# Performance work log

Measured on AMD Instinct MI355X. Metric: run time of the kernel, lower is better.

Reference implementation:

```python
import jax, jax.numpy as jnp
import numpy as np

S, T, B = 32, 64, 64          # sentences, tokens/sentence, batch
V, E, H, G, C = 32000, 128, 128, 128, 5  # vocab, embed, intra hid, inter hid, classes


def _gru_dir(x, h0, Wih, Whh, bih, bhh):
    # x: [T,B,D]; Wih: [3H,D]; Whh: [3H,H]  (PyTorch GRU gate order r,z,n)
    xg = jnp.einsum('tbd,gd->tbg', x, Wih) + bih  # precompute input gates [T,B,3H]
    def step(h, xt):
        gh = h @ Whh.T + bhh
        ir, iz, inn = jnp.split(xt, 3, axis=-1)
        hr, hz, hn = jnp.split(gh, 3, axis=-1)
        r = jax.nn.sigmoid(ir + hr)
        z = jax.nn.sigmoid(iz + hz)
        n = jnp.tanh(inn + r * hn)
        hnew = (1 - z) * n + z * h
        return hnew, hnew
    _, out = jax.lax.scan(step, h0, xg)
    return out  # [T,B,H]


def _bigru(x, Wih, Whh, bih, bhh):
    # x: [T,B,D]; Wih: [2,3H,D] (fwd, bwd). Zero initial state (init_hidden()).
    h0 = jnp.zeros((x.shape[1], Whh.shape[-1]), x.dtype)
    of = _gru_dir(x, h0, Wih[0], Whh[0], bih[0], bhh[0])
    ob = _gru_dir(x[::-1], h0, Wih[1], Whh[1], bih[1], bhh[1])[::-1]
    return jnp.concatenate([of, ob], axis=-1)  # [T,B,2H]


def setup_inputs() -> dict:
    key = jax.random.key(0)
    ks = iter(jax.random.split(key, 20))
    u = lambda k, shp, s: jax.random.uniform(k, shp, jnp.float32, -s, s)
    tokens = jax.random.randint(next(ks), (S, T, B), 0, V)
    return {
        'tokens': tokens,
        'embed_table': jax.random.normal(next(ks), (V, E), jnp.float32),
        # intra biGRU (input E, hidden H)
        'Wih_intra': u(next(ks), (2, 3 * H, E), 0.08),
        'Whh_intra': u(next(ks), (2, 3 * H, H), 0.08),
        'bih_intra': u(next(ks), (2, 3 * H), 0.08),
        'bhh_intra': u(next(ks), (2, 3 * H), 0.08),
        # intra attention
        'W_W_intra': u(next(ks), (2 * H, 2 * H), 0.1),
        'b_intra': u(next(ks), (2 * H,), 0.1),
        'proj_intra': u(next(ks), (2 * H,), 0.1),
        # inter biGRU (input 2H, hidden G)
        'Wih_inter': u(next(ks), (2, 3 * G, 2 * H), 0.08),
        'Whh_inter': u(next(ks), (2, 3 * G, G), 0.08),
        'bih_inter': u(next(ks), (2, 3 * G), 0.08),
        'bhh_inter': u(next(ks), (2, 3 * G), 0.08),
        # inter attention
        'W_W_inter': u(next(ks), (2 * G, 2 * G), 0.1),
        'b_inter': u(next(ks), (2 * G,), 0.1),
        'proj_inter': u(next(ks), (2 * G,), 0.1),
        # final linear
        'W_final': u(next(ks), (C, 2 * G), 0.06),
        'b_final': u(next(ks), (C,), 0.06),
    }


def reference(tokens, embed_table, Wih_intra, Whh_intra, bih_intra, bhh_intra,
              W_W_intra, b_intra, proj_intra, Wih_inter, Whh_inter, bih_inter,
              bhh_inter, W_W_inter, b_inter, proj_inter, W_final, b_final):
    # ---- intra (word-level) per sentence, fresh zero state each sentence ----
    emb = embed_table[tokens]                                   # [S,T,B,E]
    intra_out = jax.vmap(
        lambda xs: _bigru(xs, Wih_intra, Whh_intra, bih_intra, bhh_intra)
    )(emb)                                                      # [S,T,B,2H]
    u1 = jnp.tanh(jnp.einsum('stbh,hk->stbk', intra_out, W_W_intra) + b_intra)
    a1 = jnp.einsum('stbk,k->stb', u1, proj_intra)              # [S,T,B]
    a1 = jax.nn.softmax(a1, axis=1)                             # softmax over tokens
    sent_vecs = jnp.einsum('stb,stbh->sbh', a1, intra_out)      # [S,B,2H]
    # ---- inter (sentence-level) ----
    inter_out = _bigru(sent_vecs, Wih_inter, Whh_inter, bih_inter, bhh_inter)  # [S,B,2G]
    u2 = jnp.tanh(jnp.einsum('sbh,hk->sbk', inter_out, W_W_inter) + b_inter)
    a2 = jnp.einsum('sbk,k->sb', u2, proj_inter)                # NO softmax (faithful to source)
    doc_vec = jnp.einsum('sb,sbh->bh', a2, inter_out)           # [B,2G]
    final_map = doc_vec @ W_final.T + b_final                   # [B,C]
    return final_map
```

## Files before the change

kernel.cpp:

```cpp
#include <hip/hip_runtime.h>

#define S_ 32
#define T_ 64
#define B_ 64
#define V_ 32000
#define E_ 128
#define H_ 128
#define G_ 128
#define C_ 5

typedef short s8v __attribute__((ext_vector_type(8)));
typedef __bf16 b8v __attribute__((ext_vector_type(8)));
typedef float f32x4 __attribute__((ext_vector_type(4)));

template <typename V>
__device__ inline auto mfma_sel(V a, V b, f32x4 c, int)
    -> decltype(__builtin_amdgcn_mfma_f32_16x16x32_bf16(a, b, c, 0, 0, 0)) {
  return __builtin_amdgcn_mfma_f32_16x16x32_bf16(a, b, c, 0, 0, 0);
}
template <typename V>
__device__ inline f32x4 mfma_sel(V a, V b, f32x4 c, long) {
  return __builtin_amdgcn_mfma_f32_16x16x32_bf16(
      __builtin_bit_cast(b8v, a), __builtin_bit_cast(b8v, b), c, 0, 0, 0);
}
__device__ inline f32x4 mfma16(s8v a, s8v b, f32x4 c) { return mfma_sel(a, b, c, 0); }

__device__ inline float b2f(unsigned short u) {
  union { unsigned int i; float f; } v; v.i = ((unsigned int)u) << 16; return v.f;
}
__device__ inline unsigned short f2b(float f) {
  union { float f; unsigned int i; } v; v.f = f;
  return (unsigned short)((v.i + 0x8000u) >> 16);
}
__device__ inline unsigned short f2b_rne(float f) {
  union { float f; unsigned int i; } v; v.f = f;
  unsigned int r = (v.i + 0x7fffu + ((v.i >> 16) & 1u)) >> 16;
  return (unsigned short)r;
}
__device__ inline s8v cvt8(const float* p) {
  const float4 a = *(const float4*)p;
  const float4 b = *(const float4*)(p + 4);
  s8v r;
  r[0] = (short)f2b_rne(a.x); r[1] = (short)f2b_rne(a.y);
  r[2] = (short)f2b_rne(a.z); r[3] = (short)f2b_rne(a.w);
  r[4] = (short)f2b_rne(b.x); r[5] = (short)f2b_rne(b.y);
  r[6] = (short)f2b_rne(b.z); r[7] = (short)f2b_rne(b.w);
  return r;
}
__device__ inline float fsigm(float x) {
  return __builtin_amdgcn_rcpf(1.f + __builtin_amdgcn_exp2f(-1.44269504f * x));
}
__device__ inline float ftanh(float x) {
  return 1.f - 2.f * __builtin_amdgcn_rcpf(1.f + __builtin_amdgcn_exp2f(2.88539008f * x));
}

__device__ inline void lds_barrier() {
  asm volatile("s_waitcnt lgkmcnt(0)\n\ts_barrier" ::: "memory");
}

__global__ __launch_bounds__(256) void k_gtab(
    const float* __restrict__ emb,
    const float* __restrict__ wih,
    const float* __restrict__ bih,
    const float* __restrict__ bhh,
    const float* __restrict__ wwi,
    unsigned short* __restrict__ gtab,
    unsigned short* __restrict__ wta)
{
  __shared__ __align__(16) unsigned short smem[64 * 264];
  const int bid = blockIdx.x, tid = threadIdx.x;
  if (bid >= 3000) {
    const int n0 = (bid - 3000) * 64;
    for (int i = 0; i < 64; ++i) {
      int cid = i * 256 + tid;
      int k = cid >> 6, nl = cid & 63;
      smem[nl * 264 + k] = f2b_rne(wwi[k * 256 + n0 + nl]);
    }
    __syncthreads();
    for (int i = 0; i < 8; ++i) {
      int cid = i * 256 + tid;
      int nl = cid >> 5, k8 = cid & 31;
      *(int4*)&wta[(size_t)(n0 + nl) * 256 + k8 * 8] =
          *(const int4*)&smem[nl * 264 + k8 * 8];
    }
    return;
  }
  const int mchunk = bid / 6, nchunk = bid % 6;
  const int vbase = mchunk * 64, nbase = nchunk * 128;
  for (int i = 0; i < 8; ++i) {
    int cid = i * 256 + tid;
    int row = cid >> 5, kc = cid & 31;
    float4 v = *(const float4*)&emb[(size_t)(vbase + row) * 128 + kc * 4];
    ushort4 u;
    u.x = f2b_rne(v.x); u.y = f2b_rne(v.y); u.z = f2b_rne(v.z); u.w = f2b_rne(v.w);
    *(ushort4*)&smem[row * 136 + kc * 4] = u;
  }
  __syncthreads();
  const int w = tid >> 6, l = tid & 63, q = l >> 4, ln = l & 15;
  s8v bf[2][4];
  float bias[2];
  for (int nt = 0; nt < 2; ++nt) {
    int c = nbase + (w * 2 + nt) * 16 + ln;
    int g = (c < 384) ? c : (c - 384);
    bias[nt] = bih[c] + (g < 256 ? bhh[c] : 0.f);
    for (int kf = 0; kf < 4; ++kf)
      bf[nt][kf] = cvt8(&wih[(size_t)c * 128 + kf * 32 + q * 8]);
  }
  for (int mt = 0; mt < 4; ++mt) {
    s8v af[4];
    for (int kf = 0; kf < 4; ++kf)
      af[kf] = *(const s8v*)&smem[(mt * 16 + ln) * 136 + kf * 32 + q * 8];
    for (int nt = 0; nt < 2; ++nt) {
      f32x4 acc = {0.f, 0.f, 0.f, 0.f};
      for (int kf = 0; kf < 4; ++kf) acc = mfma16(af[kf], bf[nt][kf], acc);
      const int col = nbase + (w * 2 + nt) * 16 + ln;
      for (int r = 0; r < 4; ++r) {
        const int row = vbase + mt * 16 + q * 4 + r;
        gtab[(size_t)row * 768 + col] = f2b_rne(acc[r] + bias[nt]);
      }
    }
  }
}

__global__ __launch_bounds__(512) void k_intra(
    const int* __restrict__ tokens,
    const unsigned short* __restrict__ gtab,
    const float* __restrict__ whh,
    const float* __restrict__ bhh,
    unsigned short* __restrict__ iout)
{
  const int bid = blockIdx.x;
  const int s = bid >> 3, dir = (bid >> 2) & 1, bq = bid & 3;
  const int bbase = bq * 16;
  const int tid = threadIdx.x;
  const int w = tid >> 6, l = tid & 63, q = l >> 4, ln = l & 15;
  const int gbase = w * 16, g0 = gbase + q * 4;

  __shared__ __align__(16) unsigned short hb[2][16 * 136];
  __shared__ int tokl[T_ * 16];

  for (int i = tid; i < 2 * 16 * 136; i += 512) ((unsigned short*)hb)[i] = 0;
  for (int i = tid; i < T_ * 16; i += 512) {
    int t = i >> 4, bl = i & 15;
    tokl[i] = tokens[(s * T_ + t) * B_ + bbase + bl];
  }

  s8v af[3][4];
  float hbn[4];
  const float* whd = whh + (size_t)dir * (384 * 128);
  const float* bhd = bhh + dir * 384;
  for (int g3 = 0; g3 < 3; ++g3) {
    const int R = g3 * 128 + gbase;
    for (int kf = 0; kf < 4; ++kf)
      af[g3][kf] = cvt8(&whd[(size_t)(R + ln) * 128 + kf * 32 + q * 8]);
  }
  for (int r = 0; r < 4; ++r) hbn[r] = bhd[256 + gbase + q * 4 + r];
  float h[4] = {0.f, 0.f, 0.f, 0.f};
  const int b = bbase + ln;
  __syncthreads();

  const int tfirst = dir ? (T_ - 1) : 0;
  const unsigned short* gr0 =
      gtab + (size_t)tokl[tfirst * 16 + ln] * 768 + dir * 384 + g0;
  ushort4 xr = *(const ushort4*)&gr0[0];
  ushort4 xz = *(const ushort4*)&gr0[128];
  ushort4 xn = *(const ushort4*)&gr0[256];

  int p = 0;
  for (int step = 0; step < T_; ++step) {
    const int t = dir ? (T_ - 1 - step) : step;
    const int t1 = dir ? (t > 0 ? t - 1 : 0) : (t < T_ - 1 ? t + 1 : T_ - 1);
    const unsigned short* grn =
        gtab + (size_t)tokl[t1 * 16 + ln] * 768 + dir * 384 + g0;
    const ushort4 xrn = *(const ushort4*)&grn[0];
    const ushort4 xzn = *(const ushort4*)&grn[128];
    const ushort4 xnn = *(const ushort4*)&grn[256];

    s8v bfr[4];
    for (int kf = 0; kf < 4; ++kf)
      bfr[kf] = *(const s8v*)&hb[p][ln * 136 + kf * 32 + q * 8];
    f32x4 c0 = {0.f, 0.f, 0.f, 0.f}, c1 = c0, c2 = c0;
    for (int kf = 0; kf < 4; ++kf) {
      c0 = mfma16(af[0][kf], bfr[kf], c0);
      c1 = mfma16(af[1][kf], bfr[kf], c1);
      c2 = mfma16(af[2][kf], bfr[kf], c2);
    }

    const unsigned short* xrp = (const unsigned short*)&xr;
    const unsigned short* xzp = (const unsigned short*)&xz;
    const unsigned short* xnp = (const unsigned short*)&xn;
    unsigned short hnb[4];
    for (int r = 0; r < 4; ++r) {
      float rr = fsigm(b2f(xrp[r]) + c0[r]);
      float zz = fsigm(b2f(xzp[r]) + c1[r]);
      float nn = ftanh(b2f(xnp[r]) + rr * (c2[r] + hbn[r]));
      float hv = zz * (h[r] - nn) + nn;
      h[r] = hv;
      hnb[r] = f2b(hv);
    }
    ushort4 hv4; hv4.x = hnb[0]; hv4.y = hnb[1]; hv4.z = hnb[2]; hv4.w = hnb[3];
    *(ushort4*)&hb[p ^ 1][ln * 136 + g0] = hv4;
    *(ushort4*)&iout[((size_t)(s * T_ + t) * B_ + b) * 256 + dir * 128 + g0] = hv4;
    lds_barrier();
    p ^= 1;
    xr = xrn; xz = xzn; xn = xnn;
  }
}

__global__ __launch_bounds__(512, 1) void k_attn(
    const unsigned short* __restrict__ iout,
    const unsigned short* __restrict__ wta,
    const float* __restrict__ bint,
    const float* __restrict__ proj,
    float* __restrict__ sv)
{
  __shared__ __align__(16) unsigned short wlds[256 * 256];
  __shared__ float lgbuf[8][16];
  __shared__ float lbuf[8][8];
  const int tid = threadIdx.x, bid = blockIdx.x;
  const int s = bid >> 3, b0 = (bid & 7) * 8;
  for (int i = 0; i < 16; ++i) {
    int cid = i * 512 + tid;
    int n = cid >> 5, kc = cid & 31;
    *(int4*)&wlds[n * 256 + ((kc ^ (n & 15)) << 3)] =
        *(const int4*)&wta[(size_t)n * 256 + kc * 8];
  }
  const int w = tid >> 6, l = tid & 63, q = l >> 4, ln = l & 15;
  float bbv[16], ppv[16];
  for (int nt = 0; nt < 16; ++nt) {
    bbv[nt] = bint[nt * 16 + ln];
    ppv[nt] = proj[nt * 16 + ln];
  }
  __syncthreads();

  float O[8][8];
  for (int kf = 0; kf < 8; ++kf)
    for (int j = 0; j < 8; ++j) O[kf][j] = 0.f;
  float l_acc = 0.f;

  for (int tile = 0; tile < 4; ++tile) {
    const int t = (w * 4 + tile) * 2 + (ln >> 3);
    const size_t row = (size_t)((s * T_ + t) * B_ + b0 + (ln & 7));
    s8v af[8];
    for (int kf = 0; kf < 8; ++kf)
      af[kf] = *(const s8v*)&iout[row * 256 + kf * 32 + q * 8];
    float p0 = 0.f, p1 = 0.f, p2 = 0.f, p3 = 0.f;
    for (int nt = 0; nt < 16; ++nt) {
      f32x4 c = {0.f, 0.f, 0.f, 0.f};
      for (int kf = 0; kf < 8; ++kf) {
        s8v bf = *(const s8v*)&wlds[(nt * 16 + ln) * 256 + (((kf * 4 + q) ^ ln) << 3)];
        c = mfma16(af[kf], bf, c);
      }
      p0 += ppv[nt] * ftanh(c[0] + bbv[nt]);
      p1 += ppv[nt] * ftanh(c[1] + bbv[nt]);
      p2 += ppv[nt] * ftanh(c[2] + bbv[nt]);
      p3 += ppv[nt] * ftanh(c[3] + bbv[nt]);
    }
    for (int d = 1; d < 16; d <<= 1) {
      p0 += __shfl_xor(p0, d); p1 += __shfl_xor(p1, d);
      p2 += __shfl_xor(p2, d); p3 += __shfl_xor(p3, d);
    }
    if (ln == 0) {
      lgbuf[w][q * 4 + 0] = p0; lgbuf[w][q * 4 + 1] = p1;
      lgbuf[w][q * 4 + 2] = p2; lgbuf[w][q * 4 + 3] = p3;
    }
    const float lg = lgbuf[w][ln];
    const float e = __builtin_amdgcn_exp2f(1.44269504f * lg);
    l_acc += e;
    for (int kf = 0; kf < 8; ++kf)
      for (int j = 0; j < 8; ++j)
        O[kf][j] += e * b2f((unsigned short)af[kf][j]);
  }
  l_acc += __shfl_xor(l_acc, 8);
  for (int kf = 0; kf < 8; ++kf)
    for (int j = 0; j < 8; ++j) O[kf][j] += __shfl_xor(O[kf][j], 8);
  __syncthreads();
  float* obuf = (float*)wlds;
  if (ln < 8) {
    const int base = w * 2048 + ln * 256 + q * 8;
    for (int kf = 0; kf < 8; ++kf) {
      float4 v0; v0.x = O[kf][0]; v0.y = O[kf][1]; v0.z = O[kf][2]; v0.w = O[kf][3];
      float4 v1; v1.x = O[kf][4]; v1.y = O[kf][5]; v1.z = O[kf][6]; v1.w = O[kf][7];
      *(float4*)&obuf[base + kf * 32]     = v0;
      *(float4*)&obuf[base + kf * 32 + 4] = v1;
    }
    if (q == 0) lbuf[w][ln] = l_acc;
  }
  __syncthreads();
  const int idx = tid * 4;
  const int bb_ = idx >> 8;
  float4 acc; acc.x = 0.f; acc.y = 0.f; acc.z = 0.f; acc.w = 0.f;
  float lsum = 0.f;
  for (int w8 = 0; w8 < 8; ++w8) {
    const float4 v = *(const float4*)&obuf[w8 * 2048 + idx];
    acc.x += v.x; acc.y += v.y; acc.z += v.z; acc.w += v.w;
    lsum += lbuf[w8][bb_];
  }
  const float inv = __builtin_amdgcn_rcpf(lsum);
  float4 r; r.x = acc.x * inv; r.y = acc.y * inv; r.z = acc.z * inv; r.w = acc.w * inv;
  *(float4*)&sv[(size_t)((s * B_ + b0 + bb_) * 256) + (idx & 255)] = r;
}

__global__ __launch_bounds__(256) void k_xgi(
    const float* __restrict__ sv,
    const float* __restrict__ wihI,
    const float* __restrict__ bihI,
    const float* __restrict__ bhhI,
    float* __restrict__ xgi)
{
  const int bid = blockIdx.x, tid = threadIdx.x;
  const int r0 = bid * 8;
  __shared__ float svl[8 * 256];
  for (int i = 0; i < 8; ++i) svl[i * 256 + tid] = sv[(size_t)(r0 + i) * 256 + tid];
  __syncthreads();
  for (int cc = 0; cc < 3; ++cc) {
    const int c = cc * 256 + tid;
    const int dir = c / 384, g = c - dir * 384;
    const float bias = bihI[c] + (g < 256 ? bhhI[c] : 0.f);
    float acc[8];
    for (int i = 0; i < 8; ++i) acc[i] = bias;
    const float* wr = wihI + (size_t)c * 256;
    for (int hh = 0; hh < 256; ++hh) {
      const float wv = wr[hh];
      for (int i = 0; i < 8; ++i) acc[i] += wv * svl[i * 256 + hh];
    }
    for (int i = 0; i < 8; ++i)
      xgi[((size_t)dir * 2048 + r0 + i) * 384 + g] = acc[i];
  }
}

__global__ __launch_bounds__(512) void k_inter(
    const float* __restrict__ xgi,
    const float* __restrict__ whh,
    const float* __restrict__ bhh,
    float* __restrict__ io2)
{
  const int bid = blockIdx.x;
  const int dir = bid >> 2, bq = bid & 3, bbase = bq * 16;
  const int tid = threadIdx.x;
  const int w = tid >> 6, l = tid & 63, q = l >> 4, ln = l & 15;
  const int gbase = w * 16, g0 = gbase + q * 4;
  __shared__ __align__(16) unsigned short hb[2][16 * 136];
  for (int i = tid; i < 2 * 16 * 136; i += 512) ((unsigned short*)hb)[i] = 0;
  s8v af[3][4];
  float hbn[4];
  const float* whd = whh + (size_t)dir * (384 * 128);
  const float* bhd = bhh + dir * 384;
  for (int g3 = 0; g3 < 3; ++g3) {
    const int R = g3 * 128 + gbase;
    for (int kf = 0; kf < 4; ++kf)
      af[g3][kf] = cvt8(&whd[(size_t)(R + ln) * 128 + kf * 32 + q * 8]);
  }
  for (int r = 0; r < 4; ++r) hbn[r] = bhd[256 + gbase + q * 4 + r];
  float h[4] = {0.f, 0.f, 0.f, 0.f};
  const int b = bbase + ln;
  __syncthreads();

  const int sfirst = dir ? (S_ - 1) : 0;
  const float* xp0 = xgi + ((size_t)dir * 2048 + sfirst * 64 + b) * 384 + g0;
  float4 vr = *(const float4*)&xp0[0];
  float4 vz = *(const float4*)&xp0[128];
  float4 vn = *(const float4*)&xp0[256];

  int p = 0;
  for (int step = 0; step < S_; ++step) {
    const int sI = dir ? (S_ - 1 - step) : step;
    const int s1 = dir ? (sI > 0 ? sI - 1 : 0) : (sI < S_ - 1 ? sI + 1 : S_ - 1);
    const float* xpn = xgi + ((size_t)dir * 2048 + s1 * 64 + b) * 384 + g0;
    const float4 vrn = *(const float4*)&xpn[0];
    const float4 vzn = *(const float4*)&xpn[128];
    const float4 vnn = *(const float4*)&xpn[256];

    s8v bfr[4];
    for (int kf = 0; kf < 4; ++kf)
      bfr[kf] = *(const s8v*)&hb[p][ln * 136 + kf * 32 + q * 8];
    f32x4 c0 = {0.f, 0.f, 0.f, 0.f}, c1 = c0, c2 = c0;
    for (int kf = 0; kf < 4; ++kf) {
      c0 = mfma16(af[0][kf], bfr[kf], c0);
      c1 = mfma16(af[1][kf], bfr[kf], c1);
      c2 = mfma16(af[2][kf], bfr[kf], c2);
    }
    const float irv[4] = {vr.x, vr.y, vr.z, vr.w};
    const float izv[4] = {vz.x, vz.y, vz.z, vz.w};
    const float inv[4] = {vn.x, vn.y, vn.z, vn.w};
    unsigned short hnb[4];
    for (int r = 0; r < 4; ++r) {
      float rr = fsigm(irv[r] + c0[r]);
      float zz = fsigm(izv[r] + c1[r]);
      float nn = ftanh(inv[r] + rr * (c2[r] + hbn[r]));
      float hv = zz * (h[r] - nn) + nn;
      h[r] = hv;
      hnb[r] = f2b(hv);
    }
    ushort4 hv4; hv4.x = hnb[0]; hv4.y = hnb[1]; hv4.z = hnb[2]; hv4.w = hnb[3];
    *(ushort4*)&hb[p ^ 1][ln * 136 + g0] = hv4;
    float4 of4; of4.x = h[0]; of4.y = h[1]; of4.z = h[2]; of4.w = h[3];
    *(float4*)&io2[((size_t)(sI * 64 + b)) * 256 + dir * 128 + g0] = of4;
    lds_barrier();
    p ^= 1;
    vr = vrn; vz = vzn; vn = vnn;
  }
}

__global__ __launch_bounds__(256) void k_attn_i(
    const float* __restrict__ io2,
    const float* __restrict__ wwI,
    const float* __restrict__ bI,
    const float* __restrict__ projI,
    float* __restrict__ a2)
{
  const int bid = blockIdx.x, tid = threadIdx.x;
  const int r0 = bid * 8;
  __shared__ float iol[8 * 256];
  __shared__ float red[4 * 8];
  for (int i = 0; i < 8; ++i) iol[i * 256 + tid] = io2[(size_t)(r0 + i) * 256 + tid];
  __syncthreads();
  float acc[8];
  for (int i = 0; i < 8; ++i) acc[i] = 0.f;
  for (int hh = 0; hh < 256; ++hh) {
    const float wv = wwI[hh * 256 + tid];
    for (int i = 0; i < 8; ++i) acc[i] += wv * iol[i * 256 + hh];
  }
  const float bb = bI[tid], pp = projI[tid];
  float p[8];
  for (int i = 0; i < 8; ++i) p[i] = pp * ftanh(acc[i] + bb);
  for (int d = 1; d < 64; d <<= 1)
    for (int i = 0; i < 8; ++i) p[i] += __shfl_xor(p[i], d);
  const int w = tid >> 6, l = tid & 63;
  if (l == 0)
    for (int i = 0; i < 8; ++i) red[w * 8 + i] = p[i];
  __syncthreads();
  if (tid < 8) a2[r0 + tid] = red[tid] + red[8 + tid] + red[16 + tid] + red[24 + tid];
}

__global__ __launch_bounds__(256) void k_final(
    const float* __restrict__ a2,
    const float* __restrict__ io2,
    const float* __restrict__ wf,
    const float* __restrict__ bfi,
    float* __restrict__ out)
{
  const int b = blockIdx.x, tid = threadIdx.x;
  __shared__ float av[S_];
  __shared__ float dv[256];
  __shared__ float red[4];
  if (tid < S_) av[tid] = a2[tid * 64 + b];
  __syncthreads();
  float acc = 0.f;
  for (int s = 0; s < S_; ++s) acc += av[s] * io2[((size_t)(s * 64 + b)) * 256 + tid];
  dv[tid] = acc;
  __syncthreads();
  for (int c = 0; c < C_; ++c) {
    float pv = wf[c * 256 + tid] * dv[tid];
    for (int d = 1; d < 64; d <<= 1) pv += __shfl_xor(pv, d);
    const int w = tid >> 6, l = tid & 63;
    if (l == 0) red[w] = pv;
    __syncthreads();
    if (tid == 0)
      out[b * C_ + c] = red[0] + red[1] + red[2] + red[3] + bfi[c];
    __syncthreads();
  }
}

extern "C" void kernel_launch(void* const* d_in, const int* in_sizes, int n_in,
                              void* d_out, int out_size, void* d_ws, size_t ws_size,
                              hipStream_t stream) {
  (void)in_sizes; (void)n_in; (void)out_size; (void)ws_size;
  const int*   tokens = (const int*)d_in[0];
  const float* emb    = (const float*)d_in[1];
  const float* wih_a  = (const float*)d_in[2];
  const float* whh_a  = (const float*)d_in[3];
  const float* bih_a  = (const float*)d_in[4];
  const float* bhh_a  = (const float*)d_in[5];
  const float* ww_a   = (const float*)d_in[6];
  const float* b_a    = (const float*)d_in[7];
  const float* proj_a = (const float*)d_in[8];
  const float* wih_i  = (const float*)d_in[9];
  const float* whh_i  = (const float*)d_in[10];
  const float* bih_i  = (const float*)d_in[11];
  const float* bhh_i  = (const float*)d_in[12];
  const float* ww_i   = (const float*)d_in[13];
  const float* b_i    = (const float*)d_in[14];
  const float* proj_i = (const float*)d_in[15];
  const float* w_fin  = (const float*)d_in[16];
  const float* b_fin  = (const float*)d_in[17];

  char* ws = (char*)d_ws;
  unsigned short* gtab = (unsigned short*)(ws + 0);
  unsigned short* wta  = (unsigned short*)(ws + 49152000);
  unsigned short* iout = (unsigned short*)(ws + 49283072);
  float* sv  = (float*)(ws + 117440512);
  float* xgi = (float*)(ws + 119537664);
  float* io2 = (float*)(ws + 125829120);
  float* a2  = (float*)(ws + 127926272);

  k_gtab<<<3004, 256, 0, stream>>>(emb, wih_a, bih_a, bhh_a, ww_a, gtab, wta);
  k_intra<<<256, 512, 0, stream>>>(tokens, gtab, whh_a, bhh_a, iout);
  k_attn<<<256, 512, 0, stream>>>(iout, wta, b_a, proj_a, sv);
  k_xgi<<<256, 256, 0, stream>>>(sv, wih_i, bih_i, bhh_i, xgi);
  k_inter<<<8, 512, 0, stream>>>(xgi, whh_i, bhh_i, io2);
  k_attn_i<<<256, 256, 0, stream>>>(io2, ww_i, b_i, proj_i, a2);
  k_final<<<64, 256, 0, stream>>>(a2, io2, w_fin, b_fin, (float*)d_out);
}
```

Measured before the change: 338.5 us.

## Deepen gate prefetch in GRU recurrences and reuse embedding tile across gate chunks

The intra and inter GRU recurrences now prefetch the input-gate rows two steps ahead through a four-slot register ring, using a 4x unrolled loop. This is meant to hide the latency of the gathered gtab/xgi loads behind more than one recurrence step. Separately, k_gtab has each block load and convert its 64-row embedding tile once and loop over all six output column chunks, which cuts the grid from 3004 to 504 blocks and avoids reloading the embedding tile six times. The cost is more registers in the recurrent kernels and less parallelism in the table build.

```diff
diff --git a/kernel.cpp b/kernel.cpp
--- a/kernel.cpp
+++ b/kernel.cpp
@@ -69,8 +69,8 @@
 {
   __shared__ __align__(16) unsigned short smem[64 * 264];
   const int bid = blockIdx.x, tid = threadIdx.x;
-  if (bid >= 3000) {
-    const int n0 = (bid - 3000) * 64;
+  if (bid >= 500) {
+    const int n0 = (bid - 500) * 64;
     for (int i = 0; i < 64; ++i) {
       int cid = i * 256 + tid;
       int k = cid >> 6, nl = cid & 63;
@@ -85,8 +85,7 @@
     }
     return;
   }
-  const int mchunk = bid / 6, nchunk = bid % 6;
-  const int vbase = mchunk * 64, nbase = nchunk * 128;
+  const int vbase = bid * 64;
   for (int i = 0; i < 8; ++i) {
     int cid = i * 256 + tid;
     int row = cid >> 5, kc = cid & 31;
@@ -97,26 +96,30 @@
   }
   __syncthreads();
   const int w = tid >> 6, l = tid & 63, q = l >> 4, ln = l & 15;
-  s8v bf[2][4];
-  float bias[2];
-  for (int nt = 0; nt < 2; ++nt) {
-    int c = nbase + (w * 2 + nt) * 16 + ln;
-    int g = (c < 384) ? c : (c - 384);
-    bias[nt] = bih[c] + (g < 256 ? bhh[c] : 0.f);
+  s8v af[4][4];
+  for (int mt = 0; mt < 4; ++mt)
     for (int kf = 0; kf < 4; ++kf)
-      bf[nt][kf] = cvt8(&wih[(size_t)c * 128 + kf * 32 + q * 8]);
-  }
-  for (int mt = 0; mt < 4; ++mt) {
-    s8v af[4];
-    for (int kf = 0; kf < 4; ++kf)
-      af[kf] = *(const s8v*)&smem[(mt * 16 + ln) * 136 + kf * 32 + q * 8];
+      af[mt][kf] = *(const s8v*)&smem[(mt * 16 + ln) * 136 + kf * 32 + q * 8];
+  for (int nchunk = 0; nchunk < 6; ++nchunk) {
+    const int nbase = nchunk * 128;
+    s8v bf[2][4];
+    float bias[2];
     for (int nt = 0; nt < 2; ++nt) {
-      f32x4 acc = {0.f, 0.f, 0.f, 0.f};
-      for (int kf = 0; kf < 4; ++kf) acc = mfma16(af[kf], bf[nt][kf], acc);
-      const int col = nbase + (w * 2 + nt) * 16 + ln;
-      for (int r = 0; r < 4; ++r) {
-        const int row = vbase + mt * 16 + q * 4 + r;
-        gtab[(size_t)row * 768 + col] = f2b_rne(acc[r] + bias[nt]);
+      int c = nbase + (w * 2 + nt) * 16 + ln;
+      int g = (c < 384) ? c : (c - 384);
+      bias[nt] = bih[c] + (g < 256 ? bhh[c] : 0.f);
+      for (int kf = 0; kf < 4; ++kf)
+        bf[nt][kf] = cvt8(&wih[(size_t)c * 128 + kf * 32 + q * 8]);
+    }
+    for (int mt = 0; mt < 4; ++mt) {
+      for (int nt = 0; nt < 2; ++nt) {
+        f32x4 acc = {0.f, 0.f, 0.f, 0.f};
+        for (int kf = 0; kf < 4; ++kf) acc = mfma16(af[mt][kf], bf[nt][kf], acc);
+        const int col = nbase + (w * 2 + nt) * 16 + ln;
+        for (int r = 0; r < 4; ++r) {
+          const int row = vbase + mt * 16 + q * 4 + r;
+          gtab[(size_t)row * 768 + col] = f2b_rne(acc[r] + bias[nt]);
+        }
       }
     }
   }
@@ -159,52 +162,59 @@
   const int b = bbase + ln;
   __syncthreads();
 
-  const int tfirst = dir ? (T_ - 1) : 0;
-  const unsigned short* gr0 =
-      gtab + (size_t)tokl[tfirst * 16 + ln] * 768 + dir * 384 + g0;
-  ushort4 xr = *(const ushort4*)&gr0[0];
-  ushort4 xz = *(const ushort4*)&gr0[128];
-  ushort4 xn = *(const ushort4*)&gr0[256];
+  ushort4 Xr[4], Xz[4], Xn[4];
+#define GLOAD_I(slot, st)                                                   \
+  do {                                                                      \
+    int tt_ = (st) > (T_ - 1) ? (T_ - 1) : (st);                            \
+    int tg_ = dir ? (T_ - 1 - tt_) : tt_;                                   \
+    const unsigned short* gp_ =                                             \
+        gtab + (size_t)tokl[tg_ * 16 + ln] * 768 + dir * 384 + g0;          \
+    Xr[slot] = *(const ushort4*)&gp_[0];                                    \
+    Xz[slot] = *(const ushort4*)&gp_[128];                                  \
+    Xn[slot] = *(const ushort4*)&gp_[256];                                  \
+  } while (0)
+
+  GLOAD_I(0, 0);
+  GLOAD_I(1, 1);
 
   int p = 0;
-  for (int step = 0; step < T_; ++step) {
-    const int t = dir ? (T_ - 1 - step) : step;
-    const int t1 = dir ? (t > 0 ? t - 1 : 0) : (t < T_ - 1 ? t + 1 : T_ - 1);
-    const unsigned short* grn =
-        gtab + (size_t)tokl[t1 * 16 + ln] * 768 + dir * 384 + g0;
-    const ushort4 xrn = *(const ushort4*)&grn[0];
-    const ushort4 xzn = *(const ushort4*)&grn[128];
-    const ushort4 xnn = *(const ushort4*)&grn[256];
-
-    s8v bfr[4];
-    for (int kf = 0; kf < 4; ++kf)
-      bfr[kf] = *(const s8v*)&hb[p][ln * 136 + kf * 32 + q * 8];
-    f32x4 c0 = {0.f, 0.f, 0.f, 0.f}, c1 = c0, c2 = c0;
-    for (int kf = 0; kf < 4; ++kf) {
-      c0 = mfma16(af[0][kf], bfr[kf], c0);
-      c1 = mfma16(af[1][kf], bfr[kf], c1);
-      c2 = mfma16(af[2][kf], bfr[kf], c2);
-    }
-
-    const unsigned short* xrp = (const unsigned short*)&xr;
-    const unsigned short* xzp = (const unsigned short*)&xz;
-    const unsigned short* xnp = (const unsigned short*)&xn;
-    unsigned short hnb[4];
-    for (int r = 0; r < 4; ++r) {
-      float rr = fsigm(b2f(xrp[r]) + c0[r]);
-      float zz = fsigm(b2f(xzp[r]) + c1[r]);
-      float nn = ftanh(b2f(xnp[r]) + rr * (c2[r] + hbn[r]));
-      float hv = zz * (h[r] - nn) + nn;
-      h[r] = hv;
-      hnb[r] = f2b(hv);
-    }
-    ushort4 hv4; hv4.x = hnb[0]; hv4.y = hnb[1]; hv4.z = hnb[2]; hv4.w = hnb[3];
-    *(ushort4*)&hb[p ^ 1][ln * 136 + g0] = hv4;
-    *(ushort4*)&iout[((size_t)(s * T_ + t) * B_ + b) * 256 + dir * 128 + g0] = hv4;
-    lds_barrier();
-    p ^= 1;
-    xr = xrn; xz = xzn; xn = xnn;
-  }
+  for (int it = 0; it < T_ / 4; ++it) {
+#pragma unroll
+    for (int j = 0; j < 4; ++j) {
+      const int step = it * 4 + j;
+      const int t = dir ? (T_ - 1 - step) : step;
+      GLOAD_I((j + 2) & 3, step + 2);
+
+      s8v bfr[4];
+      for (int kf = 0; kf < 4; ++kf)
+        bfr[kf] = *(const s8v*)&hb[p][ln * 136 + kf * 32 + q * 8];
+      f32x4 c0 = {0.f, 0.f, 0.f, 0.f}, c1 = c0, c2 = c0;
+      for (int kf = 0; kf < 4; ++kf) {
+        c0 = mfma16(af[0][kf], bfr[kf], c0);
+        c1 = mfma16(af[1][kf], bfr[kf], c1);
+        c2 = mfma16(af[2][kf], bfr[kf], c2);
+      }
+
+      const unsigned short* xrp = (const unsigned short*)&Xr[j];
+      const unsigned short* xzp = (const unsigned short*)&Xz[j];
+      const unsigned short* xnp = (const unsigned short*)&Xn[j];
+      unsigned short hnb[4];
+      for (int r = 0; r < 4; ++r) {
+        float rr = fsigm(b2f(xrp[r]) + c0[r]);
+        float zz = fsigm(b2f(xzp[r]) + c1[r]);
+        float nn = ftanh(b2f(xnp[r]) + rr * (c2[r] + hbn[r]));
+        float hv = zz * (h[r] - nn) + nn;
+        h[r] = hv;
+        hnb[r] = f2b(hv);
+      }
+      ushort4 hv4; hv4.x = hnb[0]; hv4.y = hnb[1]; hv4.z = hnb[2]; hv4.w = hnb[3];
+      *(ushort4*)&hb[p ^ 1][ln * 136 + g0] = hv4;
+      *(ushort4*)&iout[((size_t)(s * T_ + t) * B_ + b) * 256 + dir * 128 + g0] = hv4;
+      lds_barrier();
+      p ^= 1;
+    }
+  }
+#undef GLOAD_I
 }
 
 __global__ __launch_bounds__(512, 1) void k_attn(
@@ -356,50 +366,58 @@
   const int b = bbase + ln;
   __syncthreads();
 
-  const int sfirst = dir ? (S_ - 1) : 0;
-  const float* xp0 = xgi + ((size_t)dir * 2048 + sfirst * 64 + b) * 384 + g0;
-  float4 vr = *(const float4*)&xp0[0];
-  float4 vz = *(const float4*)&xp0[128];
-  float4 vn = *(const float4*)&xp0[256];
+  float4 Vr[4], Vz[4], Vn[4];
+#define GLOAD_S(slot, st)                                                   \
+  do {                                                                      \
+    int tt_ = (st) > (S_ - 1) ? (S_ - 1) : (st);                            \
+    int sg_ = dir ? (S_ - 1 - tt_) : tt_;                                   \
+    const float* xp_ = xgi + ((size_t)dir * 2048 + sg_ * 64 + b) * 384 + g0;\
+    Vr[slot] = *(const float4*)&xp_[0];                                     \
+    Vz[slot] = *(const float4*)&xp_[128];                                   \
+    Vn[slot] = *(const float4*)&xp_[256];                                   \
+  } while (0)
+
+  GLOAD_S(0, 0);
+  GLOAD_S(1, 1);
 
   int p = 0;
-  for (int step = 0; step < S_; ++step) {
-    const int sI = dir ? (S_ - 1 - step) : step;
-    const int s1 = dir ? (sI > 0 ? sI - 1 : 0) : (sI < S_ - 1 ? sI + 1 : S_ - 1);
-    const float* xpn = xgi + ((size_t)dir * 2048 + s1 * 64 + b) * 384 + g0;
-    const float4 vrn = *(const float4*)&xpn[0];
-    const float4 vzn = *(const float4*)&xpn[128];
-    const float4 vnn = *(const float4*)&xpn[256];
-
-    s8v bfr[4];
-    for (int kf = 0; kf < 4; ++kf)
-      bfr[kf] = *(const s8v*)&hb[p][ln * 136 + kf * 32 + q * 8];
-    f32x4 c0 = {0.f, 0.f, 0.f, 0.f}, c1 = c0, c2 = c0;
-    for (int kf = 0; kf < 4; ++kf) {
-      c0 = mfma16(af[0][kf], bfr[kf], c0);
-      c1 = mfma16(af[1][kf], bfr[kf], c1);
-      c2 = mfma16(af[2][kf], bfr[kf], c2);
-    }
-    const float irv[4] = {vr.x, vr.y, vr.z, vr.w};
-    const float izv[4] = {vz.x, vz.y, vz.z, vz.w};
-    const float inv[4] = {vn.x, vn.y, vn.z, vn.w};
-    unsigned short hnb[4];
-    for (int r = 0; r < 4; ++r) {
-      float rr = fsigm(irv[r] + c0[r]);
-      float zz = fsigm(izv[r] + c1[r]);
-      float nn = ftanh(inv[r] + rr * (c2[r] + hbn[r]));
-      float hv = zz * (h[r] - nn) + nn;
-      h[r] = hv;
-      hnb[r] = f2b(hv);
-    }
-    ushort4 hv4; hv4.x = hnb[0]; hv4.y = hnb[1]; hv4.z = hnb[2]; hv4.w = hnb[3];
-    *(ushort4*)&hb[p ^ 1][ln * 136 + g0] = hv4;
-    float4 of4; of4.x = h[0]; of4.y = h[1]; of4.z = h[2]; of4.w = h[3];
-    *(float4*)&io2[((size_t)(sI * 64 + b)) * 256 + dir * 128 + g0] = of4;
-    lds_barrier();
-    p ^= 1;
-    vr = vrn; vz = vzn; vn = vnn;
-  }
+  for (int it = 0; it < S_ / 4; ++it) {
+#pragma unroll
+    for (int j = 0; j < 4; ++j) {
+      const int step = it * 4 + j;
+      const int sI = dir ? (S_ - 1 - step) : step;
+      GLOAD_S((j + 2) & 3, step + 2);
+
+      s8v bfr[4];
+      for (int kf = 0; kf < 4; ++kf)
+        bfr[kf] = *(const s8v*)&hb[p][ln * 136 + kf * 32 + q * 8];
+      f32x4 c0 = {0.f, 0.f, 0.f, 0.f}, c1 = c0, c2 = c0;
+      for (int kf = 0; kf < 4; ++kf) {
+        c0 = mfma16(af[0][kf], bfr[kf], c0);
+        c1 = mfma16(af[1][kf], bfr[kf], c1);
+        c2 = mfma16(af[2][kf], bfr[kf], c2);
+      }
+      const float irv[4] = {Vr[j].x, Vr[j].y, Vr[j].z, Vr[j].w};
+      const float izv[4] = {Vz[j].x, Vz[j].y, Vz[j].z, Vz[j].w};
+      const float inv[4] = {Vn[j].x, Vn[j].y, Vn[j].z, Vn[j].w};
+      unsigned short hnb[4];
+      for (int r = 0; r < 4; ++r) {
+        float rr = fsigm(irv[r] + c0[r]);
+        float zz = fsigm(izv[r] + c1[r]);
+        float nn = ftanh(inv[r] + rr * (c2[r] + hbn[r]));
+        float hv = zz * (h[r] - nn) + nn;
+        h[r] = hv;
+        hnb[r] = f2b(hv);
+      }
+      ushort4 hv4; hv4.x = hnb[0]; hv4.y = hnb[1]; hv4.z = hnb[2]; hv4.w = hnb[3];
+      *(ushort4*)&hb[p ^ 1][ln * 136 + g0] = hv4;
+      float4 of4; of4.x = h[0]; of4.y = h[1]; of4.z = h[2]; of4.w = h[3];
+      *(float4*)&io2[((size_t)(sI * 64 + b)) * 256 + dir * 128 + g0] = of4;
+      lds_barrier();
+      p ^= 1;
+    }
+  }
+#undef GLOAD_S
 }
 
 __global__ __launch_bounds__(256) void k_attn_i(
@@ -494,7 +512,7 @@
   float* io2 = (float*)(ws + 125829120);
   float* a2  = (float*)(ws + 127926272);
 
-  k_gtab<<<3004, 256, 0, stream>>>(emb, wih_a, bih_a, bhh_a, ww_a, gtab, wta);
+  k_gtab<<<504, 256, 0, stream>>>(emb, wih_a, bih_a, bhh_a, ww_a, gtab, wta);
   k_intra<<<256, 512, 0, stream>>>(tokens, gtab, whh_a, bhh_a, iout);
   k_attn<<<256, 512, 0, stream>>>(iout, wta, b_a, proj_a, sv);
   k_xgi<<<256, 256, 0, stream>>>(sv, wih_i, bih_i, bhh_i, xgi);
```

Result: faster. 311.8 us (-7.9%).
